# Kernel optimization log

Hardware: AMD Instinct MI355X
Metric: run time of the kernel (lower is better)

Reference implementation:

```python
import jax, jax.numpy as jnp
import numpy as np
import math

B, S, HID = 4, 2048, 1024
NH = 16
HD = HID // NH  # 64
DH = math.sqrt(HD)


def setup_inputs() -> dict:
    key = jax.random.key(0)
    ks = jax.random.split(key, 7)
    scale = 1.0 / math.sqrt(HID)
    return {
        "hidden_states": jax.random.normal(ks[0], (B, S, HID), dtype=jnp.float32),
        "Wq": jax.random.normal(ks[1], (HID, HID), dtype=jnp.float32) * scale,
        "bq": jnp.zeros((HID,), dtype=jnp.float32),
        "Wk": jax.random.normal(ks[2], (HID, HID), dtype=jnp.float32) * scale,
        "bk": jnp.zeros((HID,), dtype=jnp.float32),
        "Wv": jax.random.normal(ks[3], (HID, HID), dtype=jnp.float32) * scale,
        "bv": jnp.zeros((HID,), dtype=jnp.float32),
        "attention_mask": jnp.ones((B, S), dtype=jnp.int32),
    }


def _heads(x):
    # [B,S,HID] -> [B,NH,S,HD]
    b, s, _ = x.shape
    return x.reshape(b, s, NH, HD).transpose(0, 2, 1, 3)


def reference(hidden_states, Wq, bq, Wk, bk, Wv, bv, attention_mask):
    q = _heads(hidden_states @ Wq.T + bq)
    k = _heads(hidden_states @ Wk.T + bk)
    v = _heads(hidden_states @ Wv.T + bv)

    left_k = k / DH
    right_k = jax.nn.soft_sign(jax.nn.soft_sign(k) / DH) + v
    # scores: [B,NH,S,S]
    scores = jnp.einsum("bhqd,bhkd->bhqk", q, left_k + right_k) / DH
    # torch masks along the QUERY dim: mask[:, None, :, None] == 0 -> -10000
    scores = jnp.where(attention_mask[:, None, :, None] == 0, -10000.0, scores)
    probs = jax.nn.softmax(scores, axis=-1)
    ctx = jnp.einsum("bhqk,bhkd->bhqd", probs, v)
    # [B,NH,S,HD] -> [B,S,HID]
    return ctx.transpose(0, 2, 1, 3).reshape(hidden_states.shape[0], -1, HID)
```

## Files before the change

kernel.cpp:

```cpp
#include <hip/hip_runtime.h>
#include <hip/hip_fp16.h>
#include <cstdint>

#define B_   4
#define S_   2048
#define HID_ 1024
#define NH_  16
#define HD_  64
#define M_   (B_ * S_)

using f16   = _Float16;
using f16x4 = __attribute__((ext_vector_type(4))) _Float16;
using f16x8 = __attribute__((ext_vector_type(8))) _Float16;
using f32x4 = __attribute__((ext_vector_type(4))) float;
using u32x4 = __attribute__((ext_vector_type(4))) unsigned int;

__device__ __forceinline__ void g2lds16(const void* g, void* l) {
  __builtin_amdgcn_global_load_lds(
      (__attribute__((address_space(1))) void*)(uintptr_t)g,
      (__attribute__((address_space(3))) void*)(uint32_t)(uintptr_t)l,
      16, 0, 0);
}

__device__ __forceinline__ unsigned int pk16(float a, float b) {
  unsigned int r;
  asm("v_cvt_pkrtz_f16_f32 %0, %1, %2" : "=v"(r) : "v"(a), "v"(b));
  return r;
}

#define PIDX(r) (((r) & 32) | (((r) & 12) << 1) | ((((r) >> 4) & 1) << 2) | ((r) & 3))

#define CS_ 0.180336880111120426f

__global__ void cvt_all_k(const float* __restrict__ hs, const float* __restrict__ wq,
                          const float* __restrict__ wk, const float* __restrict__ wv,
                          f16* __restrict__ hsF, f16* __restrict__ wF) {
  const int bid = blockIdx.x, tid = threadIdx.x;
  const float* src;
  f16* dst;
  int i;
  if (bid < 8192) {
    src = hs; dst = hsF; i = bid * 256 + tid;
  } else {
    const int r = (bid - 8192) >> 10;
    src = (r == 0) ? wq : ((r == 1) ? wk : wv);
    dst = wF + (size_t)r * HID_ * HID_;
    i = ((bid - 8192) & 1023) * 256 + tid;
  }
  float4 v = ((const float4*)src)[i];
  f16x4 h;
  h[0] = (f16)v.x; h[1] = (f16)v.y; h[2] = (f16)v.z; h[3] = (f16)v.w;
  ((f16x4*)dst)[i] = h;
}

__global__ __launch_bounds__(256) void proj_gemm_k(
    const f16* __restrict__ A, const f16* __restrict__ W,
    const float* __restrict__ bq, const float* __restrict__ bk, const float* __restrict__ bv,
    f16* __restrict__ Out) {
  __shared__ __align__(16) f16 As[128 * 64];
  __shared__ __align__(16) f16 Bs[128 * 64];
  const int tid = threadIdx.x;
  const int l   = tid & 63;
  const int w   = tid >> 6;
  const int lr  = l & 15;
  const int lk  = (l >> 4) * 8;
  const int col0 = blockIdx.x * 128;
  const int row0 = blockIdx.y * 128;
  const int wr = (w >> 1) * 64;
  const int wc = (w & 1) * 64;

  f32x4 acc[4][4] = {};

  for (int kt = 0; kt < 16; ++kt) {
    const int k0 = kt * 64;
#pragma unroll
    for (int i = 0; i < 4; ++i) {
      const int c   = tid + i * 256;
      const int row = c >> 3;
      const int cb  = (c ^ row) & 7;
      g2lds16(A + (size_t)(row0 + row) * 1024 + k0 + cb * 8,
              As + (w * 64 + i * 256) * 8);
      g2lds16(W + (size_t)(col0 + row) * 1024 + k0 + cb * 8,
              Bs + (w * 64 + i * 256) * 8);
    }
    asm volatile("s_waitcnt vmcnt(0)" ::: "memory");
    __syncthreads();

#pragma unroll
    for (int kk = 0; kk < 64; kk += 32) {
      const int x = (kk + lk) >> 3;
      f16x8 af[4], bf[4];
#pragma unroll
      for (int m = 0; m < 4; ++m) {
        const int row = wr + m * 16 + lr;
        af[m] = *(const f16x8*)(As + (row * 8 + ((x ^ row) & 7)) * 8);
      }
#pragma unroll
      for (int n = 0; n < 4; ++n) {
        const int row = wc + n * 16 + lr;
        bf[n] = *(const f16x8*)(Bs + (row * 8 + ((x ^ row) & 7)) * 8);
      }
#pragma unroll
      for (int m = 0; m < 4; ++m)
#pragma unroll
        for (int n = 0; n < 4; ++n)
          acc[m][n] = __builtin_amdgcn_mfma_f32_16x16x32_f16(af[m], bf[n], acc[m][n], 0, 0, 0);
    }
    __syncthreads();
  }

  const int proj = col0 >> 10;
  const float* bias = (proj == 0) ? bq : ((proj == 1) ? bk : bv);
  f16* outp = Out + (size_t)proj * ((size_t)M_ * HID_);
#pragma unroll
  for (int n = 0; n < 4; ++n) {
    const int col = col0 + wc + n * 16 + lr;
    const int cp  = col & 1023;
    const float bb = bias[cp];
#pragma unroll
    for (int m = 0; m < 4; ++m) {
      const int rbase = row0 + wr + m * 16 + (l >> 4) * 4;
#pragma unroll
      for (int r = 0; r < 4; ++r)
        outp[(size_t)(rbase + r) * 1024 + cp] = (f16)(acc[m][n][r] + bb);
    }
  }
}

__global__ __launch_bounds__(256) void prep_kv_k(
    const f16* __restrict__ Kp, const f16* __restrict__ Vp,
    f16* __restrict__ Keff, f16* __restrict__ Vt) {
  const int bh = blockIdx.x;
  const int st = blockIdx.y;
  const int b = bh >> 4, h = bh & 15;
  const int tid = threadIdx.x;
#pragma unroll
  for (int i = 0; i < 2; ++i) {
    const int c  = tid + i * 256;
    const int sl = c >> 3, cb = c & 7;
    const int s  = st * 64 + sl;
    const size_t src = (size_t)(b * S_ + s) * 1024 + h * 64 + cb * 8;
    const f16x8 kv = *(const f16x8*)(Kp + src);
    const f16x8 vv = *(const f16x8*)(Vp + src);
    f16x8 ke;
#pragma unroll
    for (int j = 0; j < 8; ++j) {
      const float kf = (float)kv[j], vf = (float)vv[j];
      const float s1 = kf / (1.f + fabsf(kf));
      const float t  = s1 * 0.125f;
      const float s2 = t / (1.f + fabsf(t));
      ke[j] = (f16)((kf * 0.125f + s2 + vf) * CS_);
    }
    *(f16x8*)(Keff + ((size_t)bh * S_ + s) * 64 + cb * 8) = ke;
#pragma unroll
    for (int j = 0; j < 8; ++j)
      Vt[((size_t)bh * 64 + cb * 8 + j) * S_ + s] = vv[j];
  }
}

__global__ __launch_bounds__(512) void attn_k(
    const f16* __restrict__ Q,
    const f16* __restrict__ Keff,
    const f16* __restrict__ Vt,
    const int* __restrict__ mask,
    float* __restrict__ Out) {
  __shared__ __align__(16) f16 Kl[2][64 * 64];
  __shared__ __align__(16) f16 Vl[2][64 * 64];
  const int bh = blockIdx.x, qt = blockIdx.y;
  const int b = bh >> 4, h = bh & 15;
  const int tid = threadIdx.x;
  const int l = tid & 63, w = tid >> 6;
  const int lr = l & 15, g = l >> 4;

  f16x8 qf[2][2];
#pragma unroll
  for (int qb = 0; qb < 2; ++qb) {
    const int qrow = qt * 256 + w * 32 + qb * 16 + lr;
    const f16* qs = Q + (size_t)(b * S_ + qrow) * 1024 + h * 64 + g * 8;
    qf[qb][0] = *(const f16x8*)(qs);
    qf[qb][1] = *(const f16x8*)(qs + 32);
    if (mask[b * S_ + qrow] == 0) {
      qf[qb][0] = (f16x8)(f16)0;
      qf[qb][1] = (f16x8)(f16)0;
    }
  }

  const int srow = tid >> 3, scl = tid & 7;
  const int sc = scl ^ (srow & 7);
  const f16* kg = Keff + ((size_t)bh * S_ + PIDX(srow)) * 64 + sc * 8;
  const f16* vg = Vt + ((size_t)bh * 64 + srow) * 2048 + sc * 8;

  f32x4 ctx[2][4] = {};
  float lacc[2] = {0.f, 0.f};

#define STAGE(bf, t)                                                           \
  {                                                                            \
    g2lds16(kg + (size_t)(t) * 4096, &Kl[bf][(w * 64) * 8]);                   \
    g2lds16(vg + (size_t)(t) * 64, &Vl[bf][(w * 64) * 8]);                     \
  }

  STAGE(0, 0);
  asm volatile("s_waitcnt vmcnt(0)" ::: "memory");
  __syncthreads();

  for (int kt = 0; kt < 32; ++kt) {
    const int cur = kt & 1;
    if (kt < 31) STAGE(cur ^ 1, kt + 1);

    f16x8 pf[2][2];
#pragma unroll
    for (int cbp = 0; cbp < 2; ++cbp) {
      f32x4 sv[2][2] = {};
      __builtin_amdgcn_s_setprio(1);
#pragma unroll
      for (int kk = 0; kk < 2; ++kk)
#pragma unroll
        for (int cc = 0; cc < 2; ++cc) {
          const int row = (cbp * 2 + cc) * 16 + lr;
          const f16x8 kf = *(const f16x8*)(&Kl[cur][(row * 8 + ((kk * 4 + g) ^ (row & 7))) * 8]);
#pragma unroll
          for (int qb = 0; qb < 2; ++qb)
            sv[qb][cc] = __builtin_amdgcn_mfma_f32_16x16x32_f16(kf, qf[qb][kk], sv[qb][cc], 0, 0, 0);
        }
      __builtin_amdgcn_s_setprio(0);
#pragma unroll
      for (int qb = 0; qb < 2; ++qb) {
        float pv[2][4];
        float s = 0.f;
#pragma unroll
        for (int cc = 0; cc < 2; ++cc)
#pragma unroll
          for (int r = 0; r < 4; ++r) {
            const float pe = __builtin_amdgcn_exp2f(sv[qb][cc][r]);
            pv[cc][r] = pe;
            s += pe;
          }
        lacc[qb] += s;
        u32x4 pw = {pk16(pv[0][0], pv[0][1]), pk16(pv[0][2], pv[0][3]),
                    pk16(pv[1][0], pv[1][1]), pk16(pv[1][2], pv[1][3])};
        pf[qb][cbp] = __builtin_bit_cast(f16x8, pw);
      }
    }

    __builtin_amdgcn_s_setprio(1);
#pragma unroll
    for (int kk = 0; kk < 2; ++kk)
#pragma unroll
      for (int db = 0; db < 4; ++db) {
        const int row = db * 16 + lr;
        const f16x8 vf = *(const f16x8*)(&Vl[cur][(row * 8 + ((kk * 4 + g) ^ (row & 7))) * 8]);
#pragma unroll
        for (int qb = 0; qb < 2; ++qb)
          ctx[qb][db] = __builtin_amdgcn_mfma_f32_16x16x32_f16(vf, pf[qb][kk], ctx[qb][db], 0, 0, 0);
      }
    __builtin_amdgcn_s_setprio(0);

    asm volatile("s_waitcnt vmcnt(0)" ::: "memory");
    __syncthreads();
  }

#pragma unroll
  for (int qb = 0; qb < 2; ++qb) {
    float ls = lacc[qb];
    ls += __shfl_xor(ls, 16);
    ls += __shfl_xor(ls, 32);
    const float linv = 1.0f / ls;
    const int qrow = qt * 256 + w * 32 + qb * 16 + lr;
    float* op = Out + (size_t)(b * S_ + qrow) * 1024 + h * 64 + g * 4;
#pragma unroll
    for (int db = 0; db < 4; ++db) {
      f32x4 o = ctx[qb][db] * linv;
      *(f32x4*)(op + db * 16) = o;
    }
  }
}

extern "C" void kernel_launch(void* const* d_in, const int* in_sizes, int n_in,
                              void* d_out, int out_size, void* d_ws, size_t ws_size,
                              hipStream_t stream) {
  const float* hs = (const float*)d_in[0];
  const float* Wq = (const float*)d_in[1];
  const float* bq = (const float*)d_in[2];
  const float* Wk = (const float*)d_in[3];
  const float* bk = (const float*)d_in[4];
  const float* Wv = (const float*)d_in[5];
  const float* bv = (const float*)d_in[6];
  const int* mask = (const int*)d_in[7];
  float* out = (float*)d_out;

  f16* hsF  = (f16*)d_ws;
  f16* wF   = hsF + (size_t)M_ * HID_;
  f16* qF   = wF + 3ull * HID_ * HID_;
  f16* kF   = qF + (size_t)M_ * HID_;
  f16* vF   = kF + (size_t)M_ * HID_;
  f16* keff = vF + (size_t)M_ * HID_;
  f16* vt   = keff + (size_t)M_ * HID_;

  cvt_all_k<<<dim3(8192 + 3072), 256, 0, stream>>>(hs, Wq, Wk, Wv, hsF, wF);
  proj_gemm_k<<<dim3(24, 64), 256, 0, stream>>>(hsF, wF, bq, bk, bv, qF);
  prep_kv_k<<<dim3(64, 32), 256, 0, stream>>>(kF, vF, keff, vt);
  attn_k<<<dim3(64, 8), 512, 0, stream>>>(qF, keff, vt, mask, out);
}
```

Baseline: 165.0 us.

## Double attention key tile to 128 and swizzle projection GEMM block order

The attention kernel now stages 128 keys per iteration instead of 64, halving the number of loop iterations and barriers at the cost of twice the LDS per buffer. The V tile swizzle is widened to 16 chunks and the key permutation macro now preserves bit 6, so rows stay in the order the MFMA fragments expect. The projection GEMM uses a 1D grid with a block-index swizzle that spreads consecutive blocks across groups of 8, meant to improve L2 locality or XCD placement of shared A/W tiles. More LDS per block may reduce occupancy.

```diff
diff --git a/kernel.cpp b/kernel.cpp
--- a/kernel.cpp
+++ b/kernel.cpp
@@ -28,7 +28,7 @@
   return r;
 }
 
-#define PIDX(r) (((r) & 32) | (((r) & 12) << 1) | ((((r) >> 4) & 1) << 2) | ((r) & 3))
+#define PIDX(r) (((r) & 96) | (((r) & 12) << 1) | ((((r) >> 4) & 1) << 2) | ((r) & 3))
 
 #define CS_ 0.180336880111120426f
 
@@ -59,13 +59,16 @@
     f16* __restrict__ Out) {
   __shared__ __align__(16) f16 As[128 * 64];
   __shared__ __align__(16) f16 Bs[128 * 64];
+  const int bid = blockIdx.x;
+  const int swz = (bid & 7) * 192 + (bid >> 3);
+  const int bx = swz % 24, by = swz / 24;
   const int tid = threadIdx.x;
   const int l   = tid & 63;
   const int w   = tid >> 6;
   const int lr  = l & 15;
   const int lk  = (l >> 4) * 8;
-  const int col0 = blockIdx.x * 128;
-  const int row0 = blockIdx.y * 128;
+  const int col0 = bx * 128;
+  const int row0 = by * 128;
   const int wr = (w >> 1) * 64;
   const int wc = (w & 1) * 64;
 
@@ -164,8 +167,8 @@
     const f16* __restrict__ Vt,
     const int* __restrict__ mask,
     float* __restrict__ Out) {
-  __shared__ __align__(16) f16 Kl[2][64 * 64];
-  __shared__ __align__(16) f16 Vl[2][64 * 64];
+  __shared__ __align__(16) f16 Kl[2][128 * 64];
+  __shared__ __align__(16) f16 Vl[2][64 * 128];
   const int bh = blockIdx.x, qt = blockIdx.y;
   const int b = bh >> 4, h = bh & 15;
   const int tid = threadIdx.x;
@@ -185,31 +188,39 @@
     }
   }
 
-  const int srow = tid >> 3, scl = tid & 7;
-  const int sc = scl ^ (srow & 7);
-  const f16* kg = Keff + ((size_t)bh * S_ + PIDX(srow)) * 64 + sc * 8;
-  const f16* vg = Vt + ((size_t)bh * 64 + srow) * 2048 + sc * 8;
+  const f16* kg[2];
+  const f16* vg[2];
+#pragma unroll
+  for (int i = 0; i < 2; ++i) {
+    const int n = tid + i * 512;
+    const int krow = n >> 3, kc = (n & 7) ^ (krow & 7);
+    kg[i] = Keff + ((size_t)bh * S_ + PIDX(krow)) * 64 + kc * 8;
+    const int vrow = n >> 4, vc = (n & 15) ^ (vrow & 15);
+    vg[i] = Vt + ((size_t)bh * 64 + vrow) * 2048 + vc * 8;
+  }
 
   f32x4 ctx[2][4] = {};
   float lacc[2] = {0.f, 0.f};
 
 #define STAGE(bf, t)                                                           \
   {                                                                            \
-    g2lds16(kg + (size_t)(t) * 4096, &Kl[bf][(w * 64) * 8]);                   \
-    g2lds16(vg + (size_t)(t) * 64, &Vl[bf][(w * 64) * 8]);                     \
+    _Pragma("unroll") for (int i = 0; i < 2; ++i) {                            \
+      g2lds16(kg[i] + (size_t)(t) * 8192, &Kl[bf][(i * 512 + w * 64) * 8]);    \
+      g2lds16(vg[i] + (size_t)(t) * 128, &Vl[bf][(i * 512 + w * 64) * 8]);     \
+    }                                                                          \
   }
 
   STAGE(0, 0);
   asm volatile("s_waitcnt vmcnt(0)" ::: "memory");
   __syncthreads();
 
-  for (int kt = 0; kt < 32; ++kt) {
+  for (int kt = 0; kt < 16; ++kt) {
     const int cur = kt & 1;
-    if (kt < 31) STAGE(cur ^ 1, kt + 1);
-
-    f16x8 pf[2][2];
-#pragma unroll
-    for (int cbp = 0; cbp < 2; ++cbp) {
+    if (kt < 15) STAGE(cur ^ 1, kt + 1);
+
+    f16x8 pf[2][4];
+#pragma unroll
+    for (int cbp = 0; cbp < 4; ++cbp) {
       f32x4 sv[2][2] = {};
       __builtin_amdgcn_s_setprio(1);
 #pragma unroll
@@ -244,14 +255,14 @@
 
     __builtin_amdgcn_s_setprio(1);
 #pragma unroll
-    for (int kk = 0; kk < 2; ++kk)
+    for (int kkp = 0; kkp < 4; ++kkp)
 #pragma unroll
       for (int db = 0; db < 4; ++db) {
         const int row = db * 16 + lr;
-        const f16x8 vf = *(const f16x8*)(&Vl[cur][(row * 8 + ((kk * 4 + g) ^ (row & 7))) * 8]);
+        const f16x8 vf = *(const f16x8*)(&Vl[cur][(row * 16 + ((kkp * 4 + g) ^ (row & 15))) * 8]);
 #pragma unroll
         for (int qb = 0; qb < 2; ++qb)
-          ctx[qb][db] = __builtin_amdgcn_mfma_f32_16x16x32_f16(vf, pf[qb][kk], ctx[qb][db], 0, 0, 0);
+          ctx[qb][db] = __builtin_amdgcn_mfma_f32_16x16x32_f16(vf, pf[qb][kkp], ctx[qb][db], 0, 0, 0);
       }
     __builtin_amdgcn_s_setprio(0);
 
@@ -297,7 +308,7 @@
   f16* vt   = keff + (size_t)M_ * HID_;
 
   cvt_all_k<<<dim3(8192 + 3072), 256, 0, stream>>>(hs, Wq, Wk, Wv, hsF, wF);
-  proj_gemm_k<<<dim3(24, 64), 256, 0, stream>>>(hsF, wF, bq, bk, bv, qF);
+  proj_gemm_k<<<dim3(1536), 256, 0, stream>>>(hsF, wF, bq, bk, bv, qF);
   prep_kv_k<<<dim3(64, 32), 256, 0, stream>>>(kF, vF, keff, vt);
   attn_k<<<dim3(64, 8), 512, 0, stream>>>(qF, keff, vt, mask, out);
 }
```

Measured after the change: 169.6 us. +2.8%, slower.
